# Optimization experiments

Measured on AMD Instinct MI355X. Metric: run time of the kernel, lower is better.

The kernel has to match this reference:

```python
import jax, jax.numpy as jnp
import numpy as np

N_NODES = 50000
N_EDGES = 800000
HDIM = 128
N_RELS = 24


def setup_inputs() -> dict:
    key = jax.random.key(0)
    ks = jax.random.split(key, 7)
    h = jax.random.normal(ks[0], (N_NODES, HDIM), dtype=jnp.float32)
    # per-relation weights ('simple' regularizer: independent matrix per relation)
    W = jax.random.normal(ks[1], (N_RELS, HDIM, HDIM), dtype=jnp.float32) / np.sqrt(HDIM)
    W_loop = jax.random.normal(ks[2], (HDIM, HDIM), dtype=jnp.float32) / np.sqrt(HDIM)
    bias = jax.random.normal(ks[3], (HDIM,), dtype=jnp.float32) * 0.02
    src = jax.random.randint(ks[4], (N_EDGES,), 0, N_NODES, dtype=jnp.int32)
    dst = jax.random.randint(ks[5], (N_EDGES,), 0, N_NODES, dtype=jnp.int32)
    rel = jax.random.randint(ks[6], (N_EDGES,), 0, N_RELS, dtype=jnp.int32)
    return {"h": h, "W": W, "W_loop": W_loop, "bias": bias,
            "src": src, "dst": dst, "rel": rel}


def reference(h, W, W_loop, bias, src, dst, rel):
    """RGCN.forward(g, step=0): one RelGraphConv layer.

    msg_e  = h[src_e] @ W[rel_e]          (per-relation transform)
    agg_v  = mean_{e: dst_e = v} msg_e    (mean aggregation)
    out_v  = relu(agg_v + h_v @ W_loop + bias)   (self-loop + activation)
    skip=False, dropout=0 -> no skip-average, dropout is identity.
    """
    N, D = h.shape
    # Transform all node features by every relation matrix once: (R, N, D).
    # Then each edge gathers its (relation, source) row -- avoids gathering
    # a per-edge (E, D, D) weight tensor.
    Hr = jnp.einsum('nd,rde->rne', h, W)          # (R, N, D)
    msg = Hr[rel, src]                            # (E, D) gathered messages
    agg = jax.ops.segment_sum(msg, dst, num_segments=N)            # (N, D)
    deg = jax.ops.segment_sum(jnp.ones((msg.shape[0],), h.dtype), dst,
                              num_segments=N)                      # (N,)
    agg = agg / jnp.maximum(deg, 1.0)[:, None]    # mean aggregation
    out = jax.nn.relu(agg + h @ W_loop + bias)
    return out
```

## Files before the change

### kernel.cpp

```cpp
#include <hip/hip_runtime.h>
#include <hip/hip_bf16.h>

#define N_NODES 50000
#define N_EDGES 800000
#define HDIM    128
#define N_RELS  24

#define MAX_TILES  12524
#define SORTED_CAP (MAX_TILES * 64)
#define NSCAN_BLK  196

typedef __attribute__((ext_vector_type(8))) short bf16x8;
typedef __attribute__((ext_vector_type(4))) float f32x4;
typedef __attribute__((ext_vector_type(4))) unsigned int u32x4;

static __device__ __forceinline__ float bfbits2f(unsigned u) {
    return __uint_as_float(u << 16);
}
static __device__ __forceinline__ unsigned f2bfbits(float x) {
    union { __hip_bfloat16 b; unsigned short u; } cv;
    cv.b = __float2bfloat16(x);
    return (unsigned)cv.u;
}



__global__ void k_setup(const float* __restrict__ h,
                        const float* __restrict__ W,
                        const float* __restrict__ Wl,
                        const int* __restrict__ rel,
                        const int* __restrict__ dst,
                        unsigned short* __restrict__ hb,
                        unsigned short* __restrict__ Wbt,
                        unsigned short* __restrict__ Wlbt,
                        int* __restrict__ degi,
                        int* __restrict__ meta)
{
    __shared__ int lh[N_RELS];
    if (threadIdx.x < N_RELS) lh[threadIdx.x] = 0;
    __syncthreads();

    int stride = gridDim.x * blockDim.x;
    int tid = blockIdx.x * blockDim.x + threadIdx.x;

    const float4* h4 = (const float4*)h;
    for (int i = tid; i < N_NODES * HDIM / 4; i += stride) {
        float4 v = h4[i];
        uint2 o;
        o.x = f2bfbits(v.x) | (f2bfbits(v.y) << 16);
        o.y = f2bfbits(v.z) | (f2bfbits(v.w) << 16);
        ((uint2*)hb)[i] = o;
    }
    for (int i = tid; i < N_RELS * HDIM * HDIM / 4; i += stride) {
        int r = i >> 12, rem = i & 4095;
        int e = rem >> 5, kq = rem & 31;
        const float* wp = W + (r << 14) + (kq << 9) + e;
        uint2 o;
        o.x = f2bfbits(wp[0])   | (f2bfbits(wp[128]) << 16);
        o.y = f2bfbits(wp[256]) | (f2bfbits(wp[384]) << 16);
        ((uint2*)Wbt)[i] = o;
    }
    for (int i = tid; i < HDIM * HDIM / 4; i += stride) {
        int e = i >> 5, kq = i & 31;
        const float* wp = Wl + (kq << 9) + e;
        uint2 o;
        o.x = f2bfbits(wp[0])   | (f2bfbits(wp[128]) << 16);
        o.y = f2bfbits(wp[256]) | (f2bfbits(wp[384]) << 16);
        ((uint2*)Wlbt)[i] = o;
    }
    for (int e = tid; e < N_EDGES; e += stride) {
        atomicAdd(&lh[rel[e]], 1);
        atomicAdd(&degi[dst[e]], 1);
    }
    __syncthreads();
    if (threadIdx.x < N_RELS) atomicAdd(&meta[threadIdx.x], lh[threadIdx.x]);
}


__global__ __launch_bounds__(256) void k_bsum(const int* __restrict__ degi,
                                              int* __restrict__ bsum)
{
    int i = blockIdx.x * 256 + threadIdx.x;
    int v = (i < N_NODES) ? degi[i] : 0;
    #pragma unroll
    for (int d = 32; d > 0; d >>= 1) v += __shfl_down(v, d);
    __shared__ int ws4[4];
    int lane = threadIdx.x & 63, wv = threadIdx.x >> 6;
    if (lane == 0) ws4[wv] = v;
    __syncthreads();
    if (threadIdx.x == 0)
        bsum[blockIdx.x] = ws4[0] + ws4[1] + ws4[2] + ws4[3];
}

__global__ __launch_bounds__(256) void k_scan_misc(int* __restrict__ meta,
                                                   const int* __restrict__ bsum,
                                                   int* __restrict__ boff,
                                                   int* __restrict__ seg)
{
    __shared__ int wsum[4];
    int t = threadIdx.x;
    int v = (t < NSCAN_BLK) ? bsum[t] : 0;
    int lane = t & 63, wv = t >> 6;
    int x = v;
    #pragma unroll
    for (int d = 1; d < 64; d <<= 1) {
        int y = __shfl_up(x, d);
        if (lane >= d) x += y;
    }
    if (lane == 63) wsum[wv] = x;
    __syncthreads();
    int add = 0;
    for (int w = 0; w < wv; ++w) add += wsum[w];
    if (t < NSCAN_BLK) boff[t] = add + x - v;
    if (t == NSCAN_BLK - 1) seg[N_NODES] = add + x;

    if (t == 0) {
        int run = 0;
        for (int r = 0; r < N_RELS; ++r) {
            int cnt = meta[r];
            meta[64 + r] = run;
            meta[96 + r] = run >> 6;
            run += ((cnt + 63) >> 6) << 6;
        }
        meta[64 + N_RELS] = run;
        meta[96 + N_RELS] = run >> 6;
    }
}

__global__ __launch_bounds__(256) void k_seg(const int* __restrict__ degi,
                                             const int* __restrict__ boff,
                                             int* __restrict__ seg,
                                             int* __restrict__ cursor)
{
    int i = blockIdx.x * 256 + threadIdx.x;
    int lane = threadIdx.x & 63, wv = threadIdx.x >> 6;
    int v = (i < N_NODES) ? degi[i] : 0;
    int x = v;
    #pragma unroll
    for (int d = 1; d < 64; d <<= 1) {
        int y = __shfl_up(x, d);
        if (lane >= d) x += y;
    }
    __shared__ int wpart[4];
    if (lane == 63) wpart[wv] = x;
    __syncthreads();
    int add = 0;
    for (int w = 0; w < wv; ++w) add += wpart[w];
    int s = boff[blockIdx.x] + add + x - v;
    if (i < N_NODES) { seg[i] = s; cursor[i] = s; }
}


__global__ void k_scatter(const int* __restrict__ rel,
                          const int* __restrict__ dst,
                          int* __restrict__ meta,
                          int* __restrict__ sorted,
                          int* __restrict__ cursor,
                          int* __restrict__ slotof)
{
    __shared__ int lh[N_RELS], lb[N_RELS];
    if (threadIdx.x < N_RELS) lh[threadIdx.x] = 0;
    __syncthreads();
    int e = blockIdx.x * blockDim.x + threadIdx.x;
    int r = 0, my = 0;
    bool valid = (e < N_EDGES);
    if (valid) {
        r = rel[e];
        my = atomicAdd(&lh[r], 1);
    }
    __syncthreads();
    if (threadIdx.x < N_RELS)
        lb[threadIdx.x] = atomicAdd(&meta[32 + threadIdx.x], lh[threadIdx.x]);
    __syncthreads();
    if (valid) {
        sorted[meta[64 + r] + lb[r] + my] = e;
        slotof[e] = atomicAdd(&cursor[dst[e]], 1);
    }
}


__global__ __launch_bounds__(256) void k_edgeA(
    const unsigned short* __restrict__ hb,
    const unsigned short* __restrict__ Wbt,
    const int* __restrict__ src,
    const int* __restrict__ sorted,
    const int* __restrict__ slotof,
    const int* __restrict__ meta,
    unsigned int* __restrict__ msg)
{
    __shared__ __align__(16) unsigned char Ws[128 * 256];

    int b = blockIdx.x;
    if (b >= meta[96 + N_RELS]) return;
    int r = 0;
    while (b >= meta[96 + r + 1]) ++r;
    int lbase = (b - meta[96 + r]) << 6;
    int lim = meta[r] - lbase;
    if (lim > 64) lim = 64;

    int t = threadIdx.x;
    int lane = t & 63, wave = t >> 6;
    int l15 = lane & 15, l4 = lane >> 4;

    int arow = (wave << 4) + l15;
    int srow = 0;
    if (arow < lim) srow = src[sorted[(b << 6) + arow]];
    const char* ap = (const char*)hb + (size_t)srow * 256 + (l4 << 4);
    bf16x8 a0 = *(const bf16x8*)(ap);
    bf16x8 a1 = *(const bf16x8*)(ap + 64);
    bf16x8 a2 = *(const bf16x8*)(ap + 128);
    bf16x8 a3 = *(const bf16x8*)(ap + 192);

    {
        int row = t >> 1, half = t & 1;
        const uint4* g = (const uint4*)((const char*)Wbt + (size_t)r * 32768 + row * 256);
        unsigned sw = (row & 7) << 4;
        #pragma unroll
        for (int j = 0; j < 8; ++j) {
            int cb = (half << 7) + (j << 4);
            *(uint4*)(Ws + row * 256 + (cb ^ sw)) = g[cb >> 4];
        }
    }
    __syncthreads();

    f32x4 acc[8];
    #pragma unroll
    for (int c = 0; c < 8; ++c) acc[c] = (f32x4)0.0f;

    #pragma unroll
    for (int kk = 0; kk < 4; ++kk) {
        int kb = (kk << 6) + (l4 << 4);
        bf16x8 a = (kk == 0) ? a0 : (kk == 1) ? a1 : (kk == 2) ? a2 : a3;
        #pragma unroll
        for (int c = 0; c < 8; ++c) {
            int brow = (c << 4) + l15;
            bf16x8 bb = *(const bf16x8*)(Ws + brow * 256 + (kb ^ ((brow & 7) << 4)));
            acc[c] = __builtin_amdgcn_mfma_f32_16x16x32_bf16(a, bb, acc[c], 0, 0, 0);
        }
    }

    #pragma unroll
    for (int i = 0; i < 4; ++i) {
        int m = (wave << 4) + (l4 << 2) + i;
        if (m < lim) {
            int eid = sorted[(b << 6) + m];
            int slot = slotof[eid];
            u32x4 o;
            o.x = f2bfbits(acc[0][i]) | (f2bfbits(acc[1][i]) << 16);
            o.y = f2bfbits(acc[2][i]) | (f2bfbits(acc[3][i]) << 16);
            o.z = f2bfbits(acc[4][i]) | (f2bfbits(acc[5][i]) << 16);
            o.w = f2bfbits(acc[6][i]) | (f2bfbits(acc[7][i]) << 16);
            __builtin_nontemporal_store(o,
                (u32x4*)((char*)msg + (size_t)slot * 256 + (l15 << 4)));
        }
    }
}


__global__ __launch_bounds__(256) void k_agg(
    const unsigned int* __restrict__ msg,
    const int* __restrict__ seg,
    unsigned short* __restrict__ aggB)
{
    int wv = threadIdx.x >> 6, lane = threadIdx.x & 63;
    int n = blockIdx.x * 4 + wv;
    if (n >= N_NODES) return;
    int s0 = seg[n], s1 = seg[n + 1];
    int deg = s1 - s0;
    int l4 = lane >> 4, l15 = lane & 15;

    float acc[8] = {0, 0, 0, 0, 0, 0, 0, 0};
    const char* base = (const char*)msg + (size_t)s0 * 256;
    int nit = (deg + 3) >> 2;
    for (int it = 0; it < nit; ++it) {
        if (it * 4 + l4 < deg) {
            u32x4 v = __builtin_nontemporal_load(
                (const u32x4*)(base + (size_t)it * 1024 + lane * 16));
            acc[0] += bfbits2f(v.x & 0xffff); acc[1] += bfbits2f(v.x >> 16);
            acc[2] += bfbits2f(v.y & 0xffff); acc[3] += bfbits2f(v.y >> 16);
            acc[4] += bfbits2f(v.z & 0xffff); acc[5] += bfbits2f(v.z >> 16);
            acc[6] += bfbits2f(v.w & 0xffff); acc[7] += bfbits2f(v.w >> 16);
        }
    }
    #pragma unroll
    for (int k = 0; k < 8; ++k) {
        acc[k] += __shfl_xor(acc[k], 16);
        acc[k] += __shfl_xor(acc[k], 32);
    }
    if (l4 == 0) {
        float inv = 1.0f / fmaxf((float)deg, 1.0f);
        u32x4 u;
        u.x = f2bfbits(acc[0] * inv) | (f2bfbits(acc[1] * inv) << 16);
        u.y = f2bfbits(acc[2] * inv) | (f2bfbits(acc[3] * inv) << 16);
        u.z = f2bfbits(acc[4] * inv) | (f2bfbits(acc[5] * inv) << 16);
        u.w = f2bfbits(acc[6] * inv) | (f2bfbits(acc[7] * inv) << 16);
        *(u32x4*)((char*)aggB + (size_t)n * 256 + l15 * 16) = u;
    }
}


__global__ __launch_bounds__(256) void k_selfA(
    const unsigned short* __restrict__ hb,
    const unsigned short* __restrict__ Wlbt,
    const float* __restrict__ bias,
    const unsigned short* __restrict__ aggB,
    float* __restrict__ out)
{
    __shared__ __align__(16) unsigned char Ws[128 * 256];
    __shared__ float biasS[128];

    int b = blockIdx.x, t = threadIdx.x;
    int n0 = b << 6;
    int lane = t & 63, wave = t >> 6;
    int l15 = lane & 15, l4 = lane >> 4;

    if (t < 128) biasS[t] = bias[t];

    int arow = (wave << 4) + l15;
    int va = n0 + arow; if (va > N_NODES - 1) va = N_NODES - 1;
    const char* ap = (const char*)hb + (size_t)va * 256 + (l4 << 4);
    bf16x8 a0 = *(const bf16x8*)(ap);
    bf16x8 a1 = *(const bf16x8*)(ap + 64);
    bf16x8 a2 = *(const bf16x8*)(ap + 128);
    bf16x8 a3 = *(const bf16x8*)(ap + 192);

    {
        int row = t >> 1, half = t & 1;
        const uint4* g = (const uint4*)((const char*)Wlbt + row * 256);
        unsigned sw = (row & 7) << 4;
        #pragma unroll
        for (int j = 0; j < 8; ++j) {
            int cb = (half << 7) + (j << 4);
            *(uint4*)(Ws + row * 256 + (cb ^ sw)) = g[cb >> 4];
        }
    }
    __syncthreads();

    f32x4 acc[8];
    #pragma unroll
    for (int c = 0; c < 8; ++c) acc[c] = (f32x4)0.0f;

    #pragma unroll
    for (int kk = 0; kk < 4; ++kk) {
        int kb = (kk << 6) + (l4 << 4);
        bf16x8 a = (kk == 0) ? a0 : (kk == 1) ? a1 : (kk == 2) ? a2 : a3;
        #pragma unroll
        for (int c = 0; c < 8; ++c) {
            int brow = (c << 4) + l15;
            bf16x8 bb = *(const bf16x8*)(Ws + brow * 256 + (kb ^ ((brow & 7) << 4)));
            acc[c] = __builtin_amdgcn_mfma_f32_16x16x32_bf16(a, bb, acc[c], 0, 0, 0);
        }
    }

    #pragma unroll
    for (int c = 0; c < 8; ++c) {
        #pragma unroll
        for (int i = 0; i < 4; ++i) {
            int m = (wave << 4) + (l4 << 2) + i;
            int v = n0 + m;
            if (v < N_NODES) {
                int col = (c << 4) + l15;
                float ag = bfbits2f(aggB[(size_t)v * 128 + l15 * 8 + ((c >> 1) << 1) + (c & 1)]);
                float val = acc[c][i] + ag + biasS[col];
                out[(size_t)v * 128 + col] = fmaxf(val, 0.0f);
            }
        }
    }
}


__global__ __launch_bounds__(256) void k_edgeB(
    const unsigned short* __restrict__ hb,
    const unsigned short* __restrict__ Wbt,
    const int* __restrict__ src,
    const int* __restrict__ dst,
    const int* __restrict__ sorted,
    const int* __restrict__ meta,
    float* __restrict__ agg)
{
    __shared__ __align__(16) unsigned char Ws[128 * 256];

    int b = blockIdx.x;
    if (b >= meta[96 + N_RELS]) return;
    int r = 0;
    while (b >= meta[96 + r + 1]) ++r;
    int lbase = (b - meta[96 + r]) << 6;
    int lim = meta[r] - lbase;
    if (lim > 64) lim = 64;

    int t = threadIdx.x;
    int lane = t & 63, wave = t >> 6;
    int l15 = lane & 15, l4 = lane >> 4;

    int arow = (wave << 4) + l15;
    int srow = 0;
    if (arow < lim) srow = src[sorted[(b << 6) + arow]];
    const char* ap = (const char*)hb + (size_t)srow * 256 + (l4 << 4);
    bf16x8 a0 = *(const bf16x8*)(ap);
    bf16x8 a1 = *(const bf16x8*)(ap + 64);
    bf16x8 a2 = *(const bf16x8*)(ap + 128);
    bf16x8 a3 = *(const bf16x8*)(ap + 192);

    {
        int row = t >> 1, half = t & 1;
        const uint4* g = (const uint4*)((const char*)Wbt + (size_t)r * 32768 + row * 256);
        unsigned sw = (row & 7) << 4;
        #pragma unroll
        for (int j = 0; j < 8; ++j) {
            int cb = (half << 7) + (j << 4);
            *(uint4*)(Ws + row * 256 + (cb ^ sw)) = g[cb >> 4];
        }
    }
    __syncthreads();

    f32x4 acc[8];
    #pragma unroll
    for (int c = 0; c < 8; ++c) acc[c] = (f32x4)0.0f;

    #pragma unroll
    for (int kk = 0; kk < 4; ++kk) {
        int kb = (kk << 6) + (l4 << 4);
        bf16x8 a = (kk == 0) ? a0 : (kk == 1) ? a1 : (kk == 2) ? a2 : a3;
        #pragma unroll
        for (int c = 0; c < 8; ++c) {
            int brow = (c << 4) + l15;
            bf16x8 bb = *(const bf16x8*)(Ws + brow * 256 + (kb ^ ((brow & 7) << 4)));
            acc[c] = __builtin_amdgcn_mfma_f32_16x16x32_bf16(a, bb, acc[c], 0, 0, 0);
        }
    }

    #pragma unroll
    for (int i = 0; i < 4; ++i) {
        int m = (wave << 4) + (l4 << 2) + i;
        if (m < lim) {
            int d = dst[sorted[(b << 6) + m]];
            #pragma unroll
            for (int c = 0; c < 8; ++c)
                atomicAdd(&agg[(size_t)d * 128 + (c << 4) + l15], acc[c][i]);
        }
    }
}

__global__ __launch_bounds__(256) void k_selfB(
    const unsigned short* __restrict__ hb,
    const unsigned short* __restrict__ Wlbt,
    const float* __restrict__ bias,
    const int* __restrict__ degi,
    float* __restrict__ agg)
{
    __shared__ __align__(16) unsigned char Ws[128 * 256];
    __shared__ float biasS[128];

    int b = blockIdx.x, t = threadIdx.x;
    int n0 = b << 6;
    int lane = t & 63, wave = t >> 6;
    int l15 = lane & 15, l4 = lane >> 4;

    if (t < 128) biasS[t] = bias[t];

    int arow = (wave << 4) + l15;
    int va = n0 + arow; if (va > N_NODES - 1) va = N_NODES - 1;
    const char* ap = (const char*)hb + (size_t)va * 256 + (l4 << 4);
    bf16x8 a0 = *(const bf16x8*)(ap);
    bf16x8 a1 = *(const bf16x8*)(ap + 64);
    bf16x8 a2 = *(const bf16x8*)(ap + 128);
    bf16x8 a3 = *(const bf16x8*)(ap + 192);

    {
        int row = t >> 1, half = t & 1;
        const uint4* g = (const uint4*)((const char*)Wlbt + row * 256);
        unsigned sw = (row & 7) << 4;
        #pragma unroll
        for (int j = 0; j < 8; ++j) {
            int cb = (half << 7) + (j << 4);
            *(uint4*)(Ws + row * 256 + (cb ^ sw)) = g[cb >> 4];
        }
    }
    __syncthreads();

    f32x4 acc[8];
    #pragma unroll
    for (int c = 0; c < 8; ++c) acc[c] = (f32x4)0.0f;

    #pragma unroll
    for (int kk = 0; kk < 4; ++kk) {
        int kb = (kk << 6) + (l4 << 4);
        bf16x8 a = (kk == 0) ? a0 : (kk == 1) ? a1 : (kk == 2) ? a2 : a3;
        #pragma unroll
        for (int c = 0; c < 8; ++c) {
            int brow = (c << 4) + l15;
            bf16x8 bb = *(const bf16x8*)(Ws + brow * 256 + (kb ^ ((brow & 7) << 4)));
            acc[c] = __builtin_amdgcn_mfma_f32_16x16x32_bf16(a, bb, acc[c], 0, 0, 0);
        }
    }

    #pragma unroll
    for (int c = 0; c < 8; ++c) {
        #pragma unroll
        for (int i = 0; i < 4; ++i) {
            int m = (wave << 4) + (l4 << 2) + i;
            int v = n0 + m;
            if (v < N_NODES) {
                int col = (c << 4) + l15;
                float inv = 1.0f / fmaxf((float)degi[v], 1.0f);
                float val = acc[c][i] + agg[(size_t)v * 128 + col] * inv + biasS[col];
                agg[(size_t)v * 128 + col] = fmaxf(val, 0.0f);
            }
        }
    }
}


extern "C" void kernel_launch(void* const* d_in, const int* in_sizes, int n_in,
                              void* d_out, int out_size, void* d_ws, size_t ws_size,
                              hipStream_t stream)
{
    (void)in_sizes; (void)n_in; (void)out_size;

    const float* h    = (const float*)d_in[0];
    const float* W    = (const float*)d_in[1];
    const float* Wl   = (const float*)d_in[2];
    const float* bias = (const float*)d_in[3];
    const int*   src  = (const int*)d_in[4];
    const int*   dst  = (const int*)d_in[5];
    const int*   rel  = (const int*)d_in[6];
    float* out = (float*)d_out;

    char* ws = (char*)d_ws;
    size_t off = 0;
    auto take = [&](size_t bytes) -> char* {
        char* p = ws + off;
        off += (bytes + 255) & ~(size_t)255;
        return p;
    };
    unsigned short* hb   = (unsigned short*)take((size_t)N_NODES * HDIM * 2);
    unsigned short* Wbt  = (unsigned short*)take((size_t)N_RELS * HDIM * HDIM * 2);
    unsigned short* Wlbt = (unsigned short*)take((size_t)HDIM * HDIM * 2);
    int*   degi    = (int*)take((size_t)N_NODES * 4);
    int*   meta    = (int*)take(1024);
    int*   sorted  = (int*)take((size_t)SORTED_CAP * 4);
    int*   seg     = (int*)take((size_t)(N_NODES + 1) * 4);
    int*   cursor  = (int*)take((size_t)N_NODES * 4);
    int*   bsum    = (int*)take((size_t)NSCAN_BLK * 4);
    int*   boff    = (int*)take((size_t)NSCAN_BLK * 4);
    int*   slotof  = (int*)take((size_t)N_EDGES * 4);
    unsigned int*   msg  = (unsigned int*)take((size_t)N_EDGES * HDIM * 2);
    unsigned short* aggB = (unsigned short*)take((size_t)N_NODES * HDIM * 2);
    size_t big_need = off;

    bool pathA = (ws_size >= big_need);

    size_t zbytes = (size_t)((char*)meta - (char*)degi) + 1024;
    (void)hipMemsetAsync(degi, 0, zbytes, stream);

    k_setup<<<2048, 256, 0, stream>>>(h, W, Wl, rel, dst, hb, Wbt, Wlbt, degi, meta);
    k_bsum<<<NSCAN_BLK, 256, 0, stream>>>(degi, bsum);
    k_scan_misc<<<1, 256, 0, stream>>>(meta, bsum, boff, seg);
    k_seg<<<NSCAN_BLK, 256, 0, stream>>>(degi, boff, seg, cursor);
    k_scatter<<<(N_EDGES + 255) / 256, 256, 0, stream>>>(rel, dst, meta, sorted, cursor, slotof);

    if (pathA) {
        k_edgeA<<<MAX_TILES, 256, 0, stream>>>(hb, Wbt, src, sorted, slotof, meta, msg);
        k_agg<<<(N_NODES + 3) / 4, 256, 0, stream>>>(msg, seg, aggB);
        k_selfA<<<(N_NODES + 63) / 64, 256, 0, stream>>>(hb, Wlbt, bias, aggB, out);
    } else {
        (void)hipMemsetAsync(out, 0, (size_t)N_NODES * HDIM * 4, stream);
        k_edgeB<<<MAX_TILES, 256, 0, stream>>>(hb, Wbt, src, dst, sorted, meta, out);
        k_selfB<<<(N_NODES + 63) / 64, 256, 0, stream>>>(hb, Wlbt, bias, degi, out);
    }
}
```

Measured before the change: 373.0 us.

## Pack src and slot per sorted edge and process several tiles per block

The scatter kernel now writes an int2 (src, destination slot) at each edge's relation-sorted position. The edge kernel can then read that record directly instead of following two dependent indirections (sorted->src and sorted->slotof). The edge kernel also handles four tiles per block and reloads the relation weight matrix into LDS only when the relation changes, so the 32KB weight load is amortised. The trade-offs are a larger edinfo buffer, extra scattered writes in the scatter kernel, and fewer blocks with serialized tiles, which may reduce latency hiding.

```diff
diff --git a/kernel.cpp b/kernel.cpp
--- a/kernel.cpp
+++ b/kernel.cpp
@@ -9,6 +9,7 @@
 #define MAX_TILES  12524
 #define SORTED_CAP (MAX_TILES * 64)
 #define NSCAN_BLK  196
+#define TPB        4
 
 typedef __attribute__((ext_vector_type(8))) short bf16x8;
 typedef __attribute__((ext_vector_type(4))) float f32x4;
@@ -153,10 +154,11 @@
 
 __global__ void k_scatter(const int* __restrict__ rel,
                           const int* __restrict__ dst,
+                          const int* __restrict__ src,
                           int* __restrict__ meta,
                           int* __restrict__ sorted,
                           int* __restrict__ cursor,
-                          int* __restrict__ slotof)
+                          int2* __restrict__ edinfo)
 {
     __shared__ int lh[N_RELS], lb[N_RELS];
     if (threadIdx.x < N_RELS) lh[threadIdx.x] = 0;
@@ -173,8 +175,10 @@
         lb[threadIdx.x] = atomicAdd(&meta[32 + threadIdx.x], lh[threadIdx.x]);
     __syncthreads();
     if (valid) {
-        sorted[meta[64 + r] + lb[r] + my] = e;
-        slotof[e] = atomicAdd(&cursor[dst[e]], 1);
+        int pos = meta[64 + r] + lb[r] + my;
+        sorted[pos] = e;
+        int slot = atomicAdd(&cursor[dst[e]], 1);
+        edinfo[pos] = make_int2(src[e], slot);
     }
 }
 
@@ -182,76 +186,82 @@
 __global__ __launch_bounds__(256) void k_edgeA(
     const unsigned short* __restrict__ hb,
     const unsigned short* __restrict__ Wbt,
-    const int* __restrict__ src,
-    const int* __restrict__ sorted,
-    const int* __restrict__ slotof,
+    const int2* __restrict__ edinfo,
     const int* __restrict__ meta,
     unsigned int* __restrict__ msg)
 {
     __shared__ __align__(16) unsigned char Ws[128 * 256];
 
-    int b = blockIdx.x;
-    if (b >= meta[96 + N_RELS]) return;
-    int r = 0;
-    while (b >= meta[96 + r + 1]) ++r;
-    int lbase = (b - meta[96 + r]) << 6;
-    int lim = meta[r] - lbase;
-    if (lim > 64) lim = 64;
+    int ntiles = meta[96 + N_RELS];
+    int b0 = blockIdx.x * TPB;
+    if (b0 >= ntiles) return;
 
     int t = threadIdx.x;
     int lane = t & 63, wave = t >> 6;
     int l15 = lane & 15, l4 = lane >> 4;
 
-    int arow = (wave << 4) + l15;
-    int srow = 0;
-    if (arow < lim) srow = src[sorted[(b << 6) + arow]];
-    const char* ap = (const char*)hb + (size_t)srow * 256 + (l4 << 4);
-    bf16x8 a0 = *(const bf16x8*)(ap);
-    bf16x8 a1 = *(const bf16x8*)(ap + 64);
-    bf16x8 a2 = *(const bf16x8*)(ap + 128);
-    bf16x8 a3 = *(const bf16x8*)(ap + 192);
-
-    {
-        int row = t >> 1, half = t & 1;
-        const uint4* g = (const uint4*)((const char*)Wbt + (size_t)r * 32768 + row * 256);
-        unsigned sw = (row & 7) << 4;
-        #pragma unroll
-        for (int j = 0; j < 8; ++j) {
-            int cb = (half << 7) + (j << 4);
-            *(uint4*)(Ws + row * 256 + (cb ^ sw)) = g[cb >> 4];
-        }
-    }
-    __syncthreads();
-
-    f32x4 acc[8];
-    #pragma unroll
-    for (int c = 0; c < 8; ++c) acc[c] = (f32x4)0.0f;
-
-    #pragma unroll
-    for (int kk = 0; kk < 4; ++kk) {
-        int kb = (kk << 6) + (l4 << 4);
-        bf16x8 a = (kk == 0) ? a0 : (kk == 1) ? a1 : (kk == 2) ? a2 : a3;
-        #pragma unroll
-        for (int c = 0; c < 8; ++c) {
-            int brow = (c << 4) + l15;
-            bf16x8 bb = *(const bf16x8*)(Ws + brow * 256 + (kb ^ ((brow & 7) << 4)));
-            acc[c] = __builtin_amdgcn_mfma_f32_16x16x32_bf16(a, bb, acc[c], 0, 0, 0);
-        }
-    }
-
-    #pragma unroll
-    for (int i = 0; i < 4; ++i) {
-        int m = (wave << 4) + (l4 << 2) + i;
-        if (m < lim) {
-            int eid = sorted[(b << 6) + m];
-            int slot = slotof[eid];
-            u32x4 o;
-            o.x = f2bfbits(acc[0][i]) | (f2bfbits(acc[1][i]) << 16);
-            o.y = f2bfbits(acc[2][i]) | (f2bfbits(acc[3][i]) << 16);
-            o.z = f2bfbits(acc[4][i]) | (f2bfbits(acc[5][i]) << 16);
-            o.w = f2bfbits(acc[6][i]) | (f2bfbits(acc[7][i]) << 16);
-            __builtin_nontemporal_store(o,
-                (u32x4*)((char*)msg + (size_t)slot * 256 + (l15 << 4)));
+    int rcur = -1;
+    for (int bt = 0; bt < TPB; ++bt) {
+        int b = b0 + bt;
+        if (b >= ntiles) break;
+        int r = rcur < 0 ? 0 : rcur;
+        while (b >= meta[96 + r + 1]) ++r;
+        int lbase = (b - meta[96 + r]) << 6;
+        int lim = meta[r] - lbase;
+        if (lim > 64) lim = 64;
+
+        if (r != rcur) {
+            if (bt > 0) __syncthreads();
+            int row = t >> 1, half = t & 1;
+            const uint4* g = (const uint4*)((const char*)Wbt + (size_t)r * 32768 + row * 256);
+            unsigned sw = (row & 7) << 4;
+            #pragma unroll
+            for (int j = 0; j < 8; ++j) {
+                int cb = (half << 7) + (j << 4);
+                *(uint4*)(Ws + row * 256 + (cb ^ sw)) = g[cb >> 4];
+            }
+            rcur = r;
+            __syncthreads();
+        }
+
+        int arow = (wave << 4) + l15;
+        int srow = 0;
+        if (arow < lim) srow = edinfo[(b << 6) + arow].x;
+        const char* ap = (const char*)hb + (size_t)srow * 256 + (l4 << 4);
+        bf16x8 a0 = *(const bf16x8*)(ap);
+        bf16x8 a1 = *(const bf16x8*)(ap + 64);
+        bf16x8 a2 = *(const bf16x8*)(ap + 128);
+        bf16x8 a3 = *(const bf16x8*)(ap + 192);
+
+        f32x4 acc[8];
+        #pragma unroll
+        for (int c = 0; c < 8; ++c) acc[c] = (f32x4)0.0f;
+
+        #pragma unroll
+        for (int kk = 0; kk < 4; ++kk) {
+            int kb = (kk << 6) + (l4 << 4);
+            bf16x8 a = (kk == 0) ? a0 : (kk == 1) ? a1 : (kk == 2) ? a2 : a3;
+            #pragma unroll
+            for (int c = 0; c < 8; ++c) {
+                int brow = (c << 4) + l15;
+                bf16x8 bb = *(const bf16x8*)(Ws + brow * 256 + (kb ^ ((brow & 7) << 4)));
+                acc[c] = __builtin_amdgcn_mfma_f32_16x16x32_bf16(a, bb, acc[c], 0, 0, 0);
+            }
+        }
+
+        #pragma unroll
+        for (int i = 0; i < 4; ++i) {
+            int m = (wave << 4) + (l4 << 2) + i;
+            if (m < lim) {
+                int slot = edinfo[(b << 6) + m].y;
+                u32x4 o;
+                o.x = f2bfbits(acc[0][i]) | (f2bfbits(acc[1][i]) << 16);
+                o.y = f2bfbits(acc[2][i]) | (f2bfbits(acc[3][i]) << 16);
+                o.z = f2bfbits(acc[4][i]) | (f2bfbits(acc[5][i]) << 16);
+                o.w = f2bfbits(acc[6][i]) | (f2bfbits(acc[7][i]) << 16);
+                __builtin_nontemporal_store(o,
+                    (u32x4*)((char*)msg + (size_t)slot * 256 + (l15 << 4)));
+            }
         }
     }
 }
@@ -543,7 +553,7 @@
     int*   cursor  = (int*)take((size_t)N_NODES * 4);
     int*   bsum    = (int*)take((size_t)NSCAN_BLK * 4);
     int*   boff    = (int*)take((size_t)NSCAN_BLK * 4);
-    int*   slotof  = (int*)take((size_t)N_EDGES * 4);
+    int2*  edinfo  = (int2*)take((size_t)SORTED_CAP * 8);
     unsigned int*   msg  = (unsigned int*)take((size_t)N_EDGES * HDIM * 2);
     unsigned short* aggB = (unsigned short*)take((size_t)N_NODES * HDIM * 2);
     size_t big_need = off;
@@ -557,10 +567,10 @@
     k_bsum<<<NSCAN_BLK, 256, 0, stream>>>(degi, bsum);
     k_scan_misc<<<1, 256, 0, stream>>>(meta, bsum, boff, seg);
     k_seg<<<NSCAN_BLK, 256, 0, stream>>>(degi, boff, seg, cursor);
-    k_scatter<<<(N_EDGES + 255) / 256, 256, 0, stream>>>(rel, dst, meta, sorted, cursor, slotof);
+    k_scatter<<<(N_EDGES + 255) / 256, 256, 0, stream>>>(rel, dst, src, meta, sorted, cursor, edinfo);
 
     if (pathA) {
-        k_edgeA<<<MAX_TILES, 256, 0, stream>>>(hb, Wbt, src, sorted, slotof, meta, msg);
+        k_edgeA<<<(MAX_TILES + TPB - 1) / TPB, 256, 0, stream>>>(hb, Wbt, edinfo, meta, msg);
         k_agg<<<(N_NODES + 3) / 4, 256, 0, stream>>>(msg, seg, aggB);
         k_selfA<<<(N_NODES + 63) / 64, 256, 0, stream>>>(hb, Wlbt, bias, aggB, out);
     } else {
```

New measurement: 334.4 us. -10.4%, faster.
